# Performance work log

Measured on AMD Instinct MI355X. Metric: run time of the kernel, lower is better.

The kernel has to match this reference:

```python
import jax, jax.numpy as jnp
import numpy as np

D_MODEL = 1024
N_HEAD = 16
DPH = D_MODEL // N_HEAD
NEG = -1e18


def setup_inputs() -> dict:
    key = jax.random.key(0)
    ks = jax.random.split(key, 8)
    B, L = 4, 2048
    k = jax.random.normal(ks[0], (B, L, D_MODEL), dtype=jnp.float32)
    v = jax.random.normal(ks[1], (B, L, D_MODEL), dtype=jnp.float32)
    q = jax.random.normal(ks[2], (B, L, D_MODEL), dtype=jnp.float32)
    attn_mask = jax.random.randint(ks[3], (B, L, L), 0, 2, dtype=jnp.int32)
    query_mask = jnp.ones((B, L), dtype=jnp.float32)
    # xavier_uniform bounds
    bnd1 = float(np.sqrt(6.0 / (3 * D_MODEL + D_MODEL)))
    bnd2 = float(np.sqrt(6.0 / (2 * D_MODEL)))
    kqv_w = jax.random.uniform(ks[4], (3 * D_MODEL, D_MODEL), minval=-bnd1, maxval=bnd1, dtype=jnp.float32)
    kqv_b = jnp.zeros((3 * D_MODEL,), dtype=jnp.float32)
    fin_w = jax.random.uniform(ks[5], (D_MODEL, D_MODEL), minval=-bnd2, maxval=bnd2, dtype=jnp.float32)
    fin_b = jnp.zeros((D_MODEL,), dtype=jnp.float32)
    return {"k": k, "v": v, "q": q, "attn_mask": attn_mask, "query_mask": query_mask,
            "kqv_w": kqv_w, "kqv_b": kqv_b, "fin_w": fin_w, "fin_b": fin_b}


def _split_heads(x, B):
    # [B, L, D] -> [B, H, L, dph]
    return x.reshape(B, -1, N_HEAD, DPH).transpose(0, 2, 1, 3)


def reference(k, v, q, attn_mask, query_mask, kqv_w, kqv_b, fin_w, fin_b):
    B = k.shape[0]
    scaling = DPH ** (-0.5)
    # three separate projections from one fused weight tensor (as in original)
    kp = k @ kqv_w[0:D_MODEL, :].T + kqv_b[0:D_MODEL]
    qp = q @ kqv_w[D_MODEL:2 * D_MODEL, :].T + kqv_b[D_MODEL:2 * D_MODEL]
    vp = v @ kqv_w[2 * D_MODEL:, :].T + kqv_b[2 * D_MODEL:]
    kh = _split_heads(kp, B)
    qh = _split_heads(qp, B) * scaling
    vh = _split_heads(vp, B)
    attn = jnp.einsum('bhqd,bhkd->bhqk', qh, kh)  # [B,H,Lq,Lk]
    if attn_mask is not None:
        attn = jnp.where(attn_mask[:, None, :, :] != 0, NEG, attn)
    attn = jax.nn.softmax(attn, axis=-1)
    # dropout: identity (eval mode / deterministic reference)
    context = jnp.einsum('bhqk,bhkd->bhqd', attn, vh)
    context = context.transpose(0, 2, 1, 3).reshape(B, -1, D_MODEL)
    context = context @ fin_w.T + fin_b
    attn_avg = attn.sum(axis=1) / N_HEAD  # [B,Lq,Lk]
    if query_mask is not None:
        qm = query_mask[:, :, None]
        context = context * qm
        attn_avg = attn_avg * qm
    return (context, attn_avg)
```

## Files before the change

kernel.cpp:

```cpp
#include <hip/hip_runtime.h>
#include <stdint.h>


typedef unsigned short u16;
typedef __attribute__((ext_vector_type(8))) short short8;
typedef __attribute__((ext_vector_type(4))) short short4v;
typedef __attribute__((ext_vector_type(4))) float f32x4;
typedef __attribute__((ext_vector_type(4))) float float4v;
typedef __attribute__((ext_vector_type(2))) unsigned int uint2v;

__device__ __forceinline__ u16 f2bf(float f){
  union { float f; uint32_t i; } c; c.f = f;
  return (u16)((c.i + 0x7FFFu + ((c.i >> 16) & 1u)) >> 16);
}
__device__ __forceinline__ short8 ld8(const u16* p){ return *(const short8*)p; }
__device__ __forceinline__ uint32_t cvt_pk_bf16(float lo, float hi){
  uint32_t r;
  asm("v_cvt_pk_bf16_f32 %0, %1, %2" : "=v"(r) : "v"(lo), "v"(hi));
  return r;
}
__device__ __forceinline__ short8 ld8f(const float* p){
  const float4v a = *(const float4v*)p;
  const float4v b = *(const float4v*)(p + 4);
  union { short8 s; uint32_t u[4]; } r;
  r.u[0] = cvt_pk_bf16(a[0], a[1]);
  r.u[1] = cvt_pk_bf16(a[2], a[3]);
  r.u[2] = cvt_pk_bf16(b[0], b[1]);
  r.u[3] = cvt_pk_bf16(b[2], b[3]);
  return r.s;
}
__device__ __forceinline__ float exp2_fast(float x){
  float r; asm("v_exp_f32 %0, %1" : "=v"(r) : "v"(x)); return r;
}

#define MFMA(a,b,c) __builtin_amdgcn_mfma_f32_16x16x32_bf16((a),(b),(c),0,0,0)

__global__ void sentinel_k(float* out, float v){ out[0] = v; }

__global__ __launch_bounds__(256) void maskpack_k(const int* __restrict__ m,
                                                  uint64_t* __restrict__ bits){
  int t = blockIdx.x * 256 + threadIdx.x;
  uint64_t b = __ballot(m[t] != 0);
  if ((threadIdx.x & 63) == 0) bits[t >> 6] = b;
}

#define QLDA 40
__global__ __launch_bounds__(256) void qkv_gemm_k(
    const float* __restrict__ kin, const float* __restrict__ qin, const float* __restrict__ vin,
    const float* __restrict__ w, const float* __restrict__ bias,
    u16* __restrict__ qh, u16* __restrict__ kh, u16* __restrict__ vt)
{
  const int z = blockIdx.z;
  const float* A = (z == 0) ? kin : (z == 1) ? qin : vin;
  const float* W = w + (size_t)z * 1024 * 1024;
  const float* bs = bias + z * 1024;
  const int tileM = blockIdx.y * 128, tileN = blockIdx.x * 128;
  __shared__ __align__(16) u16 As[128 * QLDA];
  __shared__ __align__(16) u16 Bs[128 * QLDA];
  const int t = threadIdx.x, wave = t >> 6, lane = t & 63, quad = lane >> 4, mm = lane & 15;
  const int waveM = (wave >> 1) * 64, waveN = (wave & 1) * 64;
  f32x4 acc[4][4];
  #pragma unroll
  for (int i = 0; i < 4; i++)
    #pragma unroll
    for (int j = 0; j < 4; j++) acc[i][j] = (f32x4){0.f,0.f,0.f,0.f};

  for (int k0 = 0; k0 < 1024; k0 += 32){
    __syncthreads();
    #pragma unroll
    for (int i = 0; i < 2; i++){
      int ch = t + i * 256;
      int row = ch >> 2, lc = (ch & 3) * 8;
      *(short8*)&As[row * QLDA + lc] = ld8f(&A[(size_t)(tileM + row) * 1024 + k0 + lc]);
      *(short8*)&Bs[row * QLDA + lc] = ld8f(&W[(size_t)(tileN + row) * 1024 + k0 + lc]);
    }
    __syncthreads();
    short8 af[4], bf[4];
    #pragma unroll
    for (int m = 0; m < 4; m++) af[m] = *(const short8*)&As[(waveM + m * 16 + mm) * QLDA + quad * 8];
    #pragma unroll
    for (int n = 0; n < 4; n++) bf[n] = *(const short8*)&Bs[(waveN + n * 16 + mm) * QLDA + quad * 8];
    #pragma unroll
    for (int m = 0; m < 4; m++)
      #pragma unroll
      for (int n = 0; n < 4; n++)
        acc[m][n] = MFMA(af[m], bf[n], acc[m][n]);
  }
  const float scale = (z == 1) ? 0.18033688011112042f : 1.0f;
  #pragma unroll
  for (int m = 0; m < 4; m++)
    #pragma unroll
    for (int n = 0; n < 4; n++){
      int col = tileN + waveN + n * 16 + mm;
      float bv = bs[col];
      int h = col >> 6, d = col & 63;
      int row0 = tileM + waveM + m * 16 + quad * 4;
      if (z == 2){
        int bb = row0 >> 11, l0 = row0 & 2047;
        union { short4v s; uint32_t u[2]; } pk;
        pk.u[0] = cvt_pk_bf16(acc[m][n][0] + bv, acc[m][n][1] + bv);
        pk.u[1] = cvt_pk_bf16(acc[m][n][2] + bv, acc[m][n][3] + bv);
        *(short4v*)&vt[((size_t)(bb * 16 + h) * 64 + d) * 2048 + l0] = pk.s;
      } else {
        u16* dst = (z == 1) ? qh : kh;
        #pragma unroll
        for (int r = 0; r < 4; r++){
          int row = row0 + r;
          int bb = row >> 11, l = row & 2047;
          float v = (acc[m][n][r] + bv) * scale;
          dst[((size_t)(bb * 16 + h) * 2048 + l) * 64 + d] = f2bf(v);
        }
      }
    }
}

#define LDK 72
#define LDV 136
__global__ __launch_bounds__(256, 4) void flash_k(
    const u16* __restrict__ qh, const u16* __restrict__ kh, const u16* __restrict__ vt,
    const uint64_t* __restrict__ maskbits, u16* __restrict__ ctx,
    float* __restrict__ statsL)
{
  const int b = blockIdx.z, h = blockIdx.y, q0 = blockIdx.x * 64;
  const int t = threadIdx.x, wave = t >> 6, lane = t & 63, quad = lane >> 4, mm = lane & 15;
  __shared__ __align__(16) u16 Ks[128 * LDK];
  __shared__ __align__(16) u16 Vs[64 * LDV];
  const u16* qb = qh + (size_t)((b * 16 + h) * 2048) * 64;
  const u16* kb = kh + (size_t)((b * 16 + h) * 2048) * 64;
  const u16* vb = vt + (size_t)((b * 16 + h) * 64) * 2048;
  const int qrow = q0 + wave * 16 + mm;
  const short8 qa0 = ld8(&qb[qrow * 64 + quad * 8]);
  const short8 qa1 = ld8(&qb[qrow * 64 + 32 + quad * 8]);
  f32x4 O[4];
  for (int cb = 0; cb < 4; cb++) O[cb] = (f32x4){0.f,0.f,0.f,0.f};
  float lrn = 0.f;
  const uint64_t* mrow = maskbits + (size_t)(b * 2048 + qrow) * 32;

  for (int kt = 0; kt < 16; kt++){
    const int k0 = kt * 128;
    __syncthreads();
    #pragma unroll
    for (int i = 0; i < 4; i++){
      int ch = t + i * 256;
      int row = ch >> 3, c8 = (ch & 7) * 8;
      *(short8*)&Ks[row * LDK + c8] = ld8(&kb[(k0 + row) * 64 + c8]);
    }
    #pragma unroll
    for (int i = 0; i < 4; i++){
      int ch = t + i * 256;
      int row = ch >> 4, c8 = (ch & 15) * 8;
      *(short8*)&Vs[row * LDV + c8] = ld8(&vb[row * 2048 + k0 + c8]);
    }
    __syncthreads();
    f32x4 S[8];
    #pragma unroll
    for (int cb = 0; cb < 8; cb++){
      S[cb] = (f32x4){0.f,0.f,0.f,0.f};
      short8 kf0 = *(const short8*)&Ks[(cb * 16 + mm) * LDK + quad * 8];
      short8 kf1 = *(const short8*)&Ks[(cb * 16 + mm) * LDK + 32 + quad * 8];
      S[cb] = MFMA(kf0, qa0, S[cb]);
      S[cb] = MFMA(kf1, qa1, S[cb]);
    }
    const uint64_t wq0 = mrow[2 * kt]     >> (quad * 4);
    const uint64_t wq1 = mrow[2 * kt + 1] >> (quad * 4);
    #pragma unroll
    for (int cb = 0; cb < 8; cb++){
      const uint32_t bits = (uint32_t)(((cb < 4) ? wq0 : wq1) >> (16 * (cb & 3)));
      #pragma unroll
      for (int r = 0; r < 4; r++)
        if (bits & (1u << r)) S[cb][r] = -1e30f;
    }
    f32x4 s4 = (f32x4){0.f,0.f,0.f,0.f};
    #pragma unroll
    for (int cb = 0; cb < 8; cb++)
      #pragma unroll
      for (int r = 0; r < 4; r++){
        const float p = exp2_fast(S[cb][r]);
        S[cb][r] = p; s4[r] += p;
      }
    float tsum = (s4[0] + s4[1]) + (s4[2] + s4[3]);
    tsum += __shfl_xor(tsum, 16, 64);
    tsum += __shfl_xor(tsum, 32, 64);
    lrn += tsum;
    #pragma unroll
    for (int kc = 0; kc < 4; kc++){
      union { short8 s; uint32_t u[4]; } pa;
      pa.u[0] = cvt_pk_bf16(S[2 * kc][0],     S[2 * kc][1]);
      pa.u[1] = cvt_pk_bf16(S[2 * kc][2],     S[2 * kc][3]);
      pa.u[2] = cvt_pk_bf16(S[2 * kc + 1][0], S[2 * kc + 1][1]);
      pa.u[3] = cvt_pk_bf16(S[2 * kc + 1][2], S[2 * kc + 1][3]);
      #pragma unroll
      for (int cb = 0; cb < 4; cb++){
        union { short8 s; uint32_t u[4]; } vv;
        const uint2v vlo = *(const uint2v*)&Vs[(cb * 16 + mm) * LDV + kc * 32 + quad * 4];
        const uint2v vhi = *(const uint2v*)&Vs[(cb * 16 + mm) * LDV + kc * 32 + 16 + quad * 4];
        vv.u[0] = vlo[0]; vv.u[1] = vlo[1];
        vv.u[2] = vhi[0]; vv.u[3] = vhi[1];
        O[cb] = MFMA(pa.s, vv.s, O[cb]);
      }
    }
  }
  const float inv = (lrn > 0.f) ? 1.0f / lrn : 0.f;
  #pragma unroll
  for (int r = 0; r < 4; r++){
    const float invq = __shfl(inv, (lane & 48) | (quad * 4 + r), 64);
    const int qg = q0 + wave * 16 + quad * 4 + r;
    #pragma unroll
    for (int cb = 0; cb < 4; cb++)
      ctx[(size_t)(b * 2048 + qg) * 1024 + h * 64 + cb * 16 + mm] = f2bf(O[cb][r] * invq);
  }
  if (quad == 0) statsL[(b * 16 + h) * 2048 + qrow] = lrn;
}

__global__ __launch_bounds__(256) void attnavg_k(
    const u16* __restrict__ qh, const u16* __restrict__ kh,
    const uint64_t* __restrict__ maskbits, const float* __restrict__ statsL,
    const float* __restrict__ qmask, float* __restrict__ out2)
{
  const int b = blockIdx.z, q0 = blockIdx.y * 64, k0 = blockIdx.x * 64;
  const int t = threadIdx.x, wave = t >> 6, lane = t & 63, quad = lane >> 4, mm = lane & 15;
  __shared__ __align__(16) u16 Ks[64 * LDK];
  const int qrow = q0 + wave * 16 + mm;
  const float qm = qmask[b * 2048 + qrow];
  const uint64_t wq = maskbits[(size_t)(b * 2048 + qrow) * 32 + (k0 >> 6)] >> (quad * 4);
  f32x4 acc[4];
  for (int cb = 0; cb < 4; cb++) acc[cb] = (f32x4){0.f,0.f,0.f,0.f};
  const int ch0 = t, ch1 = t + 256;

  for (int h = 0; h < 16; h++){
    const u16* kb = kh + (size_t)((b * 16 + h) * 2048) * 64;
    const u16* qb = qh + (size_t)((b * 16 + h) * 2048) * 64;
    __syncthreads();
    *(short8*)&Ks[(ch0 >> 3) * LDK + (ch0 & 7) * 8] = ld8(&kb[(size_t)(k0 + (ch0 >> 3)) * 64 + (ch0 & 7) * 8]);
    *(short8*)&Ks[(ch1 >> 3) * LDK + (ch1 & 7) * 8] = ld8(&kb[(size_t)(k0 + (ch1 >> 3)) * 64 + (ch1 & 7) * 8]);
    __syncthreads();
    const short8 qa0 = ld8(&qb[(size_t)qrow * 64 + quad * 8]);
    const short8 qa1 = ld8(&qb[(size_t)qrow * 64 + 32 + quad * 8]);
    const float lh = statsL[(size_t)(b * 16 + h) * 2048 + qrow];
    f32x4 S[4];
    #pragma unroll
    for (int cb = 0; cb < 4; cb++){
      S[cb] = (f32x4){0.f,0.f,0.f,0.f};
      short8 kf0 = *(const short8*)&Ks[(cb * 16 + mm) * LDK + quad * 8];
      short8 kf1 = *(const short8*)&Ks[(cb * 16 + mm) * LDK + 32 + quad * 8];
      S[cb] = MFMA(kf0, qa0, S[cb]);
      S[cb] = MFMA(kf1, qa1, S[cb]);
    }
    const float sc = (lh > 0.f) ? 1.0f / (16.0f * lh) : 0.f;
    #pragma unroll
    for (int cb = 0; cb < 4; cb++){
      const uint32_t bits = (uint32_t)(wq >> (16 * cb));
      #pragma unroll
      for (int r = 0; r < 4; r++){
        const float s = (bits & (1u << r)) ? -1e30f : S[cb][r];
        acc[cb][r] += exp2_fast(s) * sc;
      }
    }
  }
  #pragma unroll
  for (int cb = 0; cb < 4; cb++){
    const f32x4 v = acc[cb] * qm;
    *(float4v*)&out2[(size_t)(b * 2048 + qrow) * 2048 + k0 + cb * 16 + quad * 4] = v;
  }
}

__global__ __launch_bounds__(256) void fin_gemm_k(
    const u16* __restrict__ A, const float* __restrict__ W, const float* __restrict__ bias,
    const float* __restrict__ qmask, float* __restrict__ out)
{
  const int tileM = blockIdx.y * 128, tileN = blockIdx.x * 128;
  __shared__ __align__(16) u16 As[128 * QLDA];
  __shared__ __align__(16) u16 Bs[128 * QLDA];
  const int t = threadIdx.x, wave = t >> 6, lane = t & 63, quad = lane >> 4, mm = lane & 15;
  const int waveM = (wave >> 1) * 64, waveN = (wave & 1) * 64;
  f32x4 acc[4][4];
  #pragma unroll
  for (int i = 0; i < 4; i++)
    #pragma unroll
    for (int j = 0; j < 4; j++) acc[i][j] = (f32x4){0.f,0.f,0.f,0.f};

  for (int k0 = 0; k0 < 1024; k0 += 32){
    __syncthreads();
    #pragma unroll
    for (int i = 0; i < 2; i++){
      int ch = t + i * 256;
      int row = ch >> 2, lc = (ch & 3) * 8;
      *(short8*)&As[row * QLDA + lc] = ld8(&A[(size_t)(tileM + row) * 1024 + k0 + lc]);
      *(short8*)&Bs[row * QLDA + lc] = ld8f(&W[(size_t)(tileN + row) * 1024 + k0 + lc]);
    }
    __syncthreads();
    short8 af[4], bf[4];
    #pragma unroll
    for (int m = 0; m < 4; m++) af[m] = *(const short8*)&As[(waveM + m * 16 + mm) * QLDA + quad * 8];
    #pragma unroll
    for (int n = 0; n < 4; n++) bf[n] = *(const short8*)&Bs[(waveN + n * 16 + mm) * QLDA + quad * 8];
    #pragma unroll
    for (int m = 0; m < 4; m++)
      #pragma unroll
      for (int n = 0; n < 4; n++)
        acc[m][n] = MFMA(af[m], bf[n], acc[m][n]);
  }
  #pragma unroll
  for (int m = 0; m < 4; m++)
    #pragma unroll
    for (int n = 0; n < 4; n++){
      int col = tileN + waveN + n * 16 + mm;
      float bv = bias[col];
      #pragma unroll
      for (int r = 0; r < 4; r++){
        int row = tileM + waveM + m * 16 + quad * 4 + r;
        float v = (acc[m][n][r] + bv) * qmask[row];
        out[(size_t)row * 1024 + col] = v;
      }
    }
}

extern "C" void kernel_launch(void* const* d_in, const int* in_sizes, int n_in,
                              void* d_out, int out_size, void* d_ws, size_t ws_size,
                              hipStream_t stream) {
  const float* k_in   = (const float*)d_in[0];
  const float* v_in   = (const float*)d_in[1];
  const float* q_in   = (const float*)d_in[2];
  const int*   amask  = (const int*)d_in[3];
  const float* qmask  = (const float*)d_in[4];
  const float* kqv_w  = (const float*)d_in[5];
  const float* kqv_b  = (const float*)d_in[6];
  const float* fin_w  = (const float*)d_in[7];
  const float* fin_b  = (const float*)d_in[8];
  float* out  = (float*)d_out;
  float* out2 = out + (size_t)8388608;

  const size_t WS_NEED = 36700160;
  if (ws_size < WS_NEED){
    sentinel_k<<<1, 1, 0, stream>>>(out, 1.0e6f + (float)(ws_size >> 20));
    return;
  }

  u16* qh  = (u16*)d_ws;
  u16* kh  = qh + (size_t)8388608;
  float* statsL = (float*)(kh + (size_t)8388608);
  uint64_t* maskbits = (uint64_t*)(statsL + 131072);
  u16* vt  = (u16*)out;
  u16* ctx = (u16*)out2;

  maskpack_k<<<dim3(65536), dim3(256), 0, stream>>>(amask, maskbits);
  qkv_gemm_k<<<dim3(8, 64, 3), dim3(256), 0, stream>>>(
      k_in, q_in, v_in, kqv_w, kqv_b, qh, kh, vt);
  flash_k<<<dim3(32, 16, 4), dim3(256), 0, stream>>>(
      qh, kh, vt, maskbits, ctx, statsL);
  fin_gemm_k<<<dim3(8, 64), dim3(256), 0, stream>>>(
      ctx, fin_w, fin_b, qmask, out);
  attnavg_k<<<dim3(32, 32, 4), dim3(256), 0, stream>>>(
      qh, kh, maskbits, statsL, qmask, out2);
}
```

Measured before the change: 647.1 us.

## Pre-convert QKV inputs to bf16, remap blocks for XCD locality, widen attnavg tiles

Adds a conversion kernel that writes bf16 copies of the k/q/v activations and the QKV weight into scratch space inside the output buffers. The QKV GEMM then loads bf16 directly instead of converting fp32 in every tile load. The QKV, flash and attn-avg kernels switch to 1D grids with an id remap that groups consecutive work onto the same XCD for L2 locality. attnavg now covers 128 keys per block, halving the redundant Q and statsL reloads per head. The cost is one extra pass over the fp32 inputs and extra scratch traffic, and the scratch placement depends on the output buffers being free at that point.

```diff
diff --git a/kernel.cpp b/kernel.cpp
--- a/kernel.cpp
+++ b/kernel.cpp
@@ -44,17 +44,34 @@
   if ((threadIdx.x & 63) == 0) bits[t >> 6] = b;
 }
 
+__global__ __launch_bounds__(256) void convert_k(
+    const float* __restrict__ kin, const float* __restrict__ qin,
+    const float* __restrict__ vin, const float* __restrict__ w,
+    u16* __restrict__ abf, u16* __restrict__ wbf)
+{
+  const int z = blockIdx.z;
+  const float* src = (z == 0) ? kin : (z == 1) ? qin : (z == 2) ? vin : w;
+  u16* dst = (z < 3) ? (abf + (size_t)z * 8388608) : wbf;
+  const size_t n8 = (z < 3) ? 1048576 : 393216;
+  for (size_t c = (size_t)blockIdx.x * 256 + threadIdx.x; c < n8;
+       c += (size_t)gridDim.x * 256)
+    *(short8*)&dst[c * 8] = ld8f(&src[c * 8]);
+}
+
 #define QLDA 40
 __global__ __launch_bounds__(256) void qkv_gemm_k(
-    const float* __restrict__ kin, const float* __restrict__ qin, const float* __restrict__ vin,
-    const float* __restrict__ w, const float* __restrict__ bias,
+    const u16* __restrict__ abf, const u16* __restrict__ wbf,
+    const float* __restrict__ bias,
     u16* __restrict__ qh, u16* __restrict__ kh, u16* __restrict__ vt)
 {
-  const int z = blockIdx.z;
-  const float* A = (z == 0) ? kin : (z == 1) ? qin : vin;
-  const float* W = w + (size_t)z * 1024 * 1024;
+  const int id = blockIdx.x;
+  const int nid = (id & 7) * 192 + (id >> 3);
+  const int x = nid & 7, rem = nid >> 3;
+  const int y = rem & 63, z = rem >> 6;
+  const u16* A = abf + (size_t)z * 8388608;
+  const u16* W = wbf + (size_t)z * 1048576;
   const float* bs = bias + z * 1024;
-  const int tileM = blockIdx.y * 128, tileN = blockIdx.x * 128;
+  const int tileM = y * 128, tileN = x * 128;
   __shared__ __align__(16) u16 As[128 * QLDA];
   __shared__ __align__(16) u16 Bs[128 * QLDA];
   const int t = threadIdx.x, wave = t >> 6, lane = t & 63, quad = lane >> 4, mm = lane & 15;
@@ -71,8 +88,8 @@
     for (int i = 0; i < 2; i++){
       int ch = t + i * 256;
       int row = ch >> 2, lc = (ch & 3) * 8;
-      *(short8*)&As[row * QLDA + lc] = ld8f(&A[(size_t)(tileM + row) * 1024 + k0 + lc]);
-      *(short8*)&Bs[row * QLDA + lc] = ld8f(&W[(size_t)(tileN + row) * 1024 + k0 + lc]);
+      *(short8*)&As[row * QLDA + lc] = ld8(&A[(size_t)(tileM + row) * 1024 + k0 + lc]);
+      *(short8*)&Bs[row * QLDA + lc] = ld8(&W[(size_t)(tileN + row) * 1024 + k0 + lc]);
     }
     __syncthreads();
     short8 af[4], bf[4];
@@ -121,7 +138,11 @@
     const uint64_t* __restrict__ maskbits, u16* __restrict__ ctx,
     float* __restrict__ statsL)
 {
-  const int b = blockIdx.z, h = blockIdx.y, q0 = blockIdx.x * 64;
+  const int id = blockIdx.x;
+  const int nid = (id & 7) * 256 + (id >> 3);
+  const int q0 = (nid & 31) * 64;
+  const int h  = (nid >> 5) & 15;
+  const int b  = nid >> 9;
   const int t = threadIdx.x, wave = t >> 6, lane = t & 63, quad = lane >> 4, mm = lane & 15;
   __shared__ __align__(16) u16 Ks[128 * LDK];
   __shared__ __align__(16) u16 Vs[64 * LDV];
@@ -217,48 +238,54 @@
     const uint64_t* __restrict__ maskbits, const float* __restrict__ statsL,
     const float* __restrict__ qmask, float* __restrict__ out2)
 {
-  const int b = blockIdx.z, q0 = blockIdx.y * 64, k0 = blockIdx.x * 64;
+  const int id = blockIdx.x;
+  const int nid = (id & 7) * 256 + (id >> 3);
+  const int k0 = (nid & 15) * 128;
+  const int q0 = ((nid >> 4) & 31) * 64;
+  const int b  = nid >> 9;
   const int t = threadIdx.x, wave = t >> 6, lane = t & 63, quad = lane >> 4, mm = lane & 15;
-  __shared__ __align__(16) u16 Ks[64 * LDK];
+  __shared__ __align__(16) u16 Ks[128 * LDK];
   const int qrow = q0 + wave * 16 + mm;
   const float qm = qmask[b * 2048 + qrow];
-  const uint64_t wq = maskbits[(size_t)(b * 2048 + qrow) * 32 + (k0 >> 6)] >> (quad * 4);
-  f32x4 acc[4];
-  for (int cb = 0; cb < 4; cb++) acc[cb] = (f32x4){0.f,0.f,0.f,0.f};
-  const int ch0 = t, ch1 = t + 256;
+  const uint64_t* mrow = maskbits + (size_t)(b * 2048 + qrow) * 32;
+  const uint64_t wq0 = mrow[(k0 >> 6)]     >> (quad * 4);
+  const uint64_t wq1 = mrow[(k0 >> 6) + 1] >> (quad * 4);
+  f32x4 acc[8];
+  #pragma unroll
+  for (int cb = 0; cb < 8; cb++) acc[cb] = (f32x4){0.f,0.f,0.f,0.f};
 
   for (int h = 0; h < 16; h++){
     const u16* kb = kh + (size_t)((b * 16 + h) * 2048) * 64;
     const u16* qb = qh + (size_t)((b * 16 + h) * 2048) * 64;
     __syncthreads();
-    *(short8*)&Ks[(ch0 >> 3) * LDK + (ch0 & 7) * 8] = ld8(&kb[(size_t)(k0 + (ch0 >> 3)) * 64 + (ch0 & 7) * 8]);
-    *(short8*)&Ks[(ch1 >> 3) * LDK + (ch1 & 7) * 8] = ld8(&kb[(size_t)(k0 + (ch1 >> 3)) * 64 + (ch1 & 7) * 8]);
+    #pragma unroll
+    for (int i = 0; i < 4; i++){
+      int ch = t + i * 256;
+      int row = ch >> 3, c8 = (ch & 7) * 8;
+      *(short8*)&Ks[row * LDK + c8] = ld8(&kb[(size_t)(k0 + row) * 64 + c8]);
+    }
     __syncthreads();
     const short8 qa0 = ld8(&qb[(size_t)qrow * 64 + quad * 8]);
     const short8 qa1 = ld8(&qb[(size_t)qrow * 64 + 32 + quad * 8]);
     const float lh = statsL[(size_t)(b * 16 + h) * 2048 + qrow];
-    f32x4 S[4];
-    #pragma unroll
-    for (int cb = 0; cb < 4; cb++){
-      S[cb] = (f32x4){0.f,0.f,0.f,0.f};
+    const float sc = (lh > 0.f) ? 1.0f / (16.0f * lh) : 0.f;
+    #pragma unroll
+    for (int cb = 0; cb < 8; cb++){
+      f32x4 S = (f32x4){0.f,0.f,0.f,0.f};
       short8 kf0 = *(const short8*)&Ks[(cb * 16 + mm) * LDK + quad * 8];
       short8 kf1 = *(const short8*)&Ks[(cb * 16 + mm) * LDK + 32 + quad * 8];
-      S[cb] = MFMA(kf0, qa0, S[cb]);
-      S[cb] = MFMA(kf1, qa1, S[cb]);
-    }
-    const float sc = (lh > 0.f) ? 1.0f / (16.0f * lh) : 0.f;
-    #pragma unroll
-    for (int cb = 0; cb < 4; cb++){
-      const uint32_t bits = (uint32_t)(wq >> (16 * cb));
+      S = MFMA(kf0, qa0, S);
+      S = MFMA(kf1, qa1, S);
+      const uint32_t bits = (uint32_t)(((cb < 4) ? wq0 : wq1) >> (16 * (cb & 3)));
       #pragma unroll
       for (int r = 0; r < 4; r++){
-        const float s = (bits & (1u << r)) ? -1e30f : S[cb][r];
+        const float s = (bits & (1u << r)) ? -1e30f : S[r];
         acc[cb][r] += exp2_fast(s) * sc;
       }
     }
   }
   #pragma unroll
-  for (int cb = 0; cb < 4; cb++){
+  for (int cb = 0; cb < 8; cb++){
     const f32x4 v = acc[cb] * qm;
     *(float4v*)&out2[(size_t)(b * 2048 + qrow) * 2048 + k0 + cb * 16 + quad * 4] = v;
   }
@@ -341,15 +368,19 @@
   float* statsL = (float*)(kh + (size_t)8388608);
   uint64_t* maskbits = (uint64_t*)(statsL + 131072);
   u16* vt  = (u16*)out;
+  u16* wbf = (u16*)(out + (size_t)4194304);
   u16* ctx = (u16*)out2;
+  u16* abf = (u16*)(out2 + (size_t)4194304);
 
   maskpack_k<<<dim3(65536), dim3(256), 0, stream>>>(amask, maskbits);
-  qkv_gemm_k<<<dim3(8, 64, 3), dim3(256), 0, stream>>>(
-      k_in, q_in, v_in, kqv_w, kqv_b, qh, kh, vt);
-  flash_k<<<dim3(32, 16, 4), dim3(256), 0, stream>>>(
+  convert_k<<<dim3(1024, 1, 4), dim3(256), 0, stream>>>(
+      k_in, q_in, v_in, kqv_w, abf, wbf);
+  qkv_gemm_k<<<dim3(1536), dim3(256), 0, stream>>>(
+      abf, wbf, kqv_b, qh, kh, vt);
+  flash_k<<<dim3(2048), dim3(256), 0, stream>>>(
       qh, kh, vt, maskbits, ctx, statsL);
   fin_gemm_k<<<dim3(8, 64), dim3(256), 0, stream>>>(
       ctx, fin_w, fin_b, qmask, out);
-  attnavg_k<<<dim3(32, 32, 4), dim3(256), 0, stream>>>(
+  attnavg_k<<<dim3(2048), dim3(256), 0, stream>>>(
       qh, kh, maskbits, statsL, qmask, out2);
 }
```

Result: faster. 621.1 us (-4.0%).
